# Performance work log

Hardware: AMD Instinct MI355X
Metric: run time of the kernel (lower is better)

The kernel has to match this reference:

```python
import jax, jax.numpy as jnp
import numpy as np

VOC_SHAPE = (100, 100, 100)   # m_k factors of voc_size = 1_000_000
EMB_SHAPE = (4, 4, 8)         # n_k factors of emb_size = 128
RANK = 16
PAD_IDX = 0
VOC = int(np.prod(VOC_SHAPE))
EMB = int(np.prod(EMB_SHAPE))


def setup_inputs() -> dict:
    key = jax.random.key(0)
    k0, k1, k2, kx = jax.random.split(key, 4)
    # TT-matrix cores [r_k, m_k, n_k, r_{k+1}], boundary ranks = 1.
    # Per-core std chosen so the reconstructed table has stddev near
    # target_stddev = sqrt(2/voc_size) (the 'nn' init intent); exact init
    # distribution is irrelevant to the math being tested.
    d = 3
    target_std = np.sqrt(2.0 / VOC)
    core_std = float((target_std / RANK ** ((d - 1) / 2.0)) ** (1.0 / d))
    core0 = jax.random.normal(k0, (1, VOC_SHAPE[0], EMB_SHAPE[0], RANK), jnp.float32) * core_std
    core1 = jax.random.normal(k1, (RANK, VOC_SHAPE[1], EMB_SHAPE[1], RANK), jnp.float32) * core_std
    core2 = jax.random.normal(k2, (RANK, VOC_SHAPE[2], EMB_SHAPE[2], 1), jnp.float32) * core_std
    x = jax.random.randint(kx, (64, 512), 0, VOC, dtype=jnp.int64)
    return {"x": x, "core0": core0, "core1": core1, "core2": core2}


def _tt_full(core0, core1, core2):
    # Sequential TT-matrix contraction, as in sample_full():
    # res accumulates shape (m1*n1*...*mk*nk, r_{k+1})
    res = core0.reshape(-1, core0.shape[-1])                      # (m1*n1, r1)
    res = res @ core1.reshape(core1.shape[0], -1)                 # (m1*n1, m2*n2*r2)
    res = res.reshape(-1, core2.shape[0]) @ core2.reshape(core2.shape[0], -1)
    # (m1, n1, m2, n2, m3, n3) -> (m1, m2, m3, n1, n2, n3) -> (VOC, EMB)
    m1, m2, m3 = VOC_SHAPE
    n1, n2, n3 = EMB_SHAPE
    full = res.reshape(m1, n1, m2, n2, m3, n3)
    full = full.transpose(0, 2, 4, 1, 3, 5).reshape(VOC, EMB)
    return full


def reference(x, core0, core1, core2):
    xshape = x.shape
    x_flat = x.reshape(-1)
    full = _tt_full(core0, core1, core2)          # [VOC, EMB] materialized table
    rows = full[x_flat]                           # gather [B*S, EMB]
    rows = jnp.where(x_flat[:, None] != PAD_IDX, rows, jnp.zeros_like(rows))
    return rows.reshape(*xshape, EMB)
```

## Files before the change

kernel.cpp:

```cpp
#include <hip/hip_runtime.h>


#define MS_STRIDE 12
#define LDS_PER_WAVE (64 * MS_STRIDE)

__global__ __launch_bounds__(256) void tt_embed_kernel(
    const int* __restrict__ x,
    const float* __restrict__ c0,
    const float* __restrict__ c1,
    const float* __restrict__ c2,
    float* __restrict__ out,
    int nTok)
{
    __shared__ __align__(16) float lds[4 * LDS_PER_WAVE];
    const int wave = threadIdx.x >> 6;
    const int lane = threadIdx.x & 63;
    const int t = blockIdx.x * 4 + wave;
    const bool active = (t < nTok);

    float* Ms = lds + wave * LDS_PER_WAVE;

    int idx = 0;
    if (active) idx = x[t];
    idx = __builtin_amdgcn_readfirstlane(idx);
    const int i1 = idx / 10000;
    const int rem = idx - i1 * 10000;
    const int i2 = rem / 100;
    const int i3 = rem - i2 * 100;

    const int r1 = lane >> 2;
    const int j2 = lane & 3;
    const float4* bp = (const float4*)(c1 + ((r1 * 100 + i2) * 4 + j2) * 16);
    float4 b0 = bp[0], b1 = bp[1], b2 = bp[2], b3 = bp[3];

    const int e0 = lane * 2;
    const int j1 = e0 >> 5;
    const int mcol = e0 & 31;
    const float4* ap = (const float4*)(c0 + i1 * 64 + j1 * 16);
    float4 a0 = ap[0], a1 = ap[1], a2 = ap[2], a3 = ap[3];

    float bb[16] = { b0.x,b0.y,b0.z,b0.w, b1.x,b1.y,b1.z,b1.w,
                     b2.x,b2.y,b2.z,b2.w, b3.x,b3.y,b3.z,b3.w };

    float mv[8];
    #pragma unroll
    for (int j = 0; j < 8; ++j) mv[j] = 0.0f;
    const float* Cb = c2 + i3 * 8;
    #pragma unroll
    for (int r2 = 0; r2 < 16; ++r2) {
        const float* cp = Cb + r2 * 800;
        const float b = bb[r2];
        mv[0] += b * cp[0]; mv[1] += b * cp[1]; mv[2] += b * cp[2]; mv[3] += b * cp[3];
        mv[4] += b * cp[4]; mv[5] += b * cp[5]; mv[6] += b * cp[6]; mv[7] += b * cp[7];
    }

    {
        float4* mp = (float4*)(Ms + lane * MS_STRIDE);
        mp[0] = make_float4(mv[0], mv[1], mv[2], mv[3]);
        mp[1] = make_float4(mv[4], mv[5], mv[6], mv[7]);
    }

    asm volatile("s_waitcnt lgkmcnt(0)" ::: "memory");

    float av[16] = { a0.x,a0.y,a0.z,a0.w, a1.x,a1.y,a1.z,a1.w,
                     a2.x,a2.y,a2.z,a2.w, a3.x,a3.y,a3.z,a3.w };

    const int rbase = (mcol >> 3) * MS_STRIDE + (mcol & 7);
    float o0 = 0.0f, o1 = 0.0f;
    #pragma unroll
    for (int r = 0; r < 16; ++r) {
        const float2 m = *(const float2*)(Ms + r * (4 * MS_STRIDE) + rbase);
        o0 += av[r] * m.x;
        o1 += av[r] * m.y;
    }

    if (idx == 0) { o0 = 0.0f; o1 = 0.0f; }

    if (active) {
        *(float2*)(out + (long)t * 128 + e0) = make_float2(o0, o1);
    }
}

extern "C" void kernel_launch(void* const* d_in, const int* in_sizes, int n_in,
                              void* d_out, int out_size, void* d_ws, size_t ws_size,
                              hipStream_t stream) {
    const int*   x  = (const int*)d_in[0];
    const float* c0 = (const float*)d_in[1];
    const float* c1 = (const float*)d_in[2];
    const float* c2 = (const float*)d_in[3];
    float* out = (float*)d_out;

    const int nTok = out_size / 128;
    const int blocks = (nTok + 3) / 4;
    tt_embed_kernel<<<dim3(blocks), dim3(256), 0, stream>>>(x, c0, c1, c2, out, nTok);
}
```

Baseline: 77.56 us.

## Reorder TT contraction to compute core0×core1 first, then core2

Changes the contraction order. Each lane now computes four entries of the core0·core1 product (j1, j2, r2), indexed by lane over the (j2, r2) pairs of core1 with 16 strided loads, and stages them in a small LDS buffer. Each lane then reads its 16-element AB row and dots it with a float2 slice of core2 to produce two outputs. This shrinks the LDS footprint and replaces the 8-wide middle accumulation. The cost is scalar-strided global loads from core1 and redundant core0 reads across lanes.

Result: slower. 85.10 us (+9.7%).

```diff
diff --git a/kernel.cpp b/kernel.cpp
--- a/kernel.cpp
+++ b/kernel.cpp
@@ -1,8 +1,8 @@
 #include <hip/hip_runtime.h>
 
 
-#define MS_STRIDE 12
-#define LDS_PER_WAVE (64 * MS_STRIDE)
+#define AB_STRIDE 68
+#define LDS_PER_WAVE (4 * AB_STRIDE)
 
 __global__ __launch_bounds__(256) void tt_embed_kernel(
     const int* __restrict__ x,
@@ -18,7 +18,7 @@
     const int t = blockIdx.x * 4 + wave;
     const bool active = (t < nTok);
 
-    float* Ms = lds + wave * LDS_PER_WAVE;
+    float* ABs = lds + wave * LDS_PER_WAVE;
 
     int idx = 0;
     if (active) idx = x[t];
@@ -28,55 +28,53 @@
     const int i2 = rem / 100;
     const int i3 = rem - i2 * 100;
 
-    const int r1 = lane >> 2;
-    const int j2 = lane & 3;
-    const float4* bp = (const float4*)(c1 + ((r1 * 100 + i2) * 4 + j2) * 16);
-    float4 b0 = bp[0], b1 = bp[1], b2 = bp[2], b3 = bp[3];
+    const float* cA = c0 + i1 * 64;
+    const float* Bb = c1 + i2 * 64 + lane;
 
-    const int e0 = lane * 2;
-    const int j1 = e0 >> 5;
-    const int mcol = e0 & 31;
-    const float4* ap = (const float4*)(c0 + i1 * 64 + j1 * 16);
-    float4 a0 = ap[0], a1 = ap[1], a2 = ap[2], a3 = ap[3];
+    float ab0 = 0.f, ab1 = 0.f, ab2 = 0.f, ab3 = 0.f;
+    #pragma unroll
+    for (int r1 = 0; r1 < 16; ++r1) {
+        const float b = Bb[r1 * 6400];
+        ab0 += cA[r1]      * b;
+        ab1 += cA[16 + r1] * b;
+        ab2 += cA[32 + r1] * b;
+        ab3 += cA[48 + r1] * b;
+    }
 
-    float bb[16] = { b0.x,b0.y,b0.z,b0.w, b1.x,b1.y,b1.z,b1.w,
-                     b2.x,b2.y,b2.z,b2.w, b3.x,b3.y,b3.z,b3.w };
+    ABs[0 * AB_STRIDE + lane] = ab0;
+    ABs[1 * AB_STRIDE + lane] = ab1;
+    ABs[2 * AB_STRIDE + lane] = ab2;
+    ABs[3 * AB_STRIDE + lane] = ab3;
 
-    float mv[8];
-    #pragma unroll
-    for (int j = 0; j < 8; ++j) mv[j] = 0.0f;
-    const float* Cb = c2 + i3 * 8;
+    const int j3 = (lane & 3) * 2;
+    const float* Cb = c2 + i3 * 8 + j3;
+    float cvx[16], cvy[16];
     #pragma unroll
     for (int r2 = 0; r2 < 16; ++r2) {
-        const float* cp = Cb + r2 * 800;
-        const float b = bb[r2];
-        mv[0] += b * cp[0]; mv[1] += b * cp[1]; mv[2] += b * cp[2]; mv[3] += b * cp[3];
-        mv[4] += b * cp[4]; mv[5] += b * cp[5]; mv[6] += b * cp[6]; mv[7] += b * cp[7];
-    }
-
-    {
-        float4* mp = (float4*)(Ms + lane * MS_STRIDE);
-        mp[0] = make_float4(mv[0], mv[1], mv[2], mv[3]);
-        mp[1] = make_float4(mv[4], mv[5], mv[6], mv[7]);
+        const float2 cv = *(const float2*)(Cb + r2 * 800);
+        cvx[r2] = cv.x; cvy[r2] = cv.y;
     }
 
     asm volatile("s_waitcnt lgkmcnt(0)" ::: "memory");
 
-    float av[16] = { a0.x,a0.y,a0.z,a0.w, a1.x,a1.y,a1.z,a1.w,
-                     a2.x,a2.y,a2.z,a2.w, a3.x,a3.y,a3.z,a3.w };
+    const int j1w = lane >> 4;
+    const int j2w = (lane >> 2) & 3;
+    const float4* abp = (const float4*)(ABs + j1w * AB_STRIDE + j2w * 16);
+    float4 q0 = abp[0], q1 = abp[1], q2 = abp[2], q3 = abp[3];
+    float ab[16] = { q0.x,q0.y,q0.z,q0.w, q1.x,q1.y,q1.z,q1.w,
+                     q2.x,q2.y,q2.z,q2.w, q3.x,q3.y,q3.z,q3.w };
 
-    const int rbase = (mcol >> 3) * MS_STRIDE + (mcol & 7);
-    float o0 = 0.0f, o1 = 0.0f;
+    float o0 = 0.f, o1 = 0.f;
     #pragma unroll
-    for (int r = 0; r < 16; ++r) {
-        const float2 m = *(const float2*)(Ms + r * (4 * MS_STRIDE) + rbase);
-        o0 += av[r] * m.x;
-        o1 += av[r] * m.y;
+    for (int r2 = 0; r2 < 16; ++r2) {
+        o0 += ab[r2] * cvx[r2];
+        o1 += ab[r2] * cvy[r2];
     }
 
-    if (idx == 0) { o0 = 0.0f; o1 = 0.0f; }
+    if (idx == 0) { o0 = 0.f; o1 = 0.f; }
 
     if (active) {
+        const int e0 = lane * 2;
         *(float2*)(out + (long)t * 128 + e0) = make_float2(o0, o1);
     }
 }
```
